# Performance work log

Measured on AMD Instinct MI355X. Metric: run time of the kernel, lower is better.

## Reference

```python
import jax, jax.numpy as jnp
import numpy as np

# PDELayer config (matches torch defaults)
Nx, Ny = 48, 48
Lx, Ly = 1.0, 1.0
T, dt = 0.01, 0.001
dx, dy = Lx / Nx, Ly / Ny
Nt = int(T / dt)  # 10 sequential stencil steps
B = 16384


def setup_inputs() -> dict:
    key = jax.random.key(0)
    u0 = jax.random.normal(key, (B, 1, Nx, Ny), dtype=jnp.float32)
    alpha_w = jnp.array([0.1, 0.1, 0.1], dtype=jnp.float32)  # alpha_w1..3
    beta_w = jnp.array([0.3, 0.2, 0.2], dtype=jnp.float32)   # beta_w1..3
    return {"u0": u0, "alpha_w": alpha_w, "beta_w": beta_w}


def _coeff_grids(alpha_w, beta_w):
    x = jnp.linspace(0.0, Lx, Nx, dtype=jnp.float32)
    y = jnp.linspace(0.0, Ly, Ny, dtype=jnp.float32)
    yy, xx = jnp.meshgrid(y, x, indexing='ij')  # [Ny, Nx]
    two_pi = jnp.float32(2.0 * np.pi)
    alpha_grid = 0.5 * dt * (alpha_w[0]
                             + alpha_w[1] * jnp.sin(two_pi * yy)
                             + alpha_w[2] * jnp.sin(2.0 * two_pi * yy)) / dx ** 2
    beta_grid = dt * (beta_w[0]
                      + beta_w[1] * jnp.cos(two_pi * xx)
                      + beta_w[2] * jnp.cos(2.0 * two_pi * xx)) / dy ** 2
    return alpha_grid[None], beta_grid[None]  # [1, Nx, Ny] (Nx==Ny)


def reference(u0, alpha_w, beta_w):
    alpha_grid, beta_grid = _coeff_grids(alpha_w, beta_w)
    # reflect-pad once; boundary ring stays frozen during time stepping
    u = jnp.pad(u0[:, 0], ((0, 0), (1, 1), (1, 1)), mode='reflect')  # [B, Nx+2, Ny+2]

    def step(u, _):
        ui = u[:, 1:-1, 1:-1]
        u_xx = u[:, 2:, 1:-1] - 2.0 * ui + u[:, :-2, 1:-1]
        u_yy = u[:, 1:-1, 2:] - 2.0 * ui + u[:, 1:-1, :-2]
        u = u.at[:, 1:-1, 1:-1].set(ui + alpha_grid * u_xx + beta_grid * u_yy)
        return u, None

    u, _ = jax.lax.scan(step, u, None, length=Nt)
    return u[:, 1:-1, 1:-1][:, None]  # [B, 1, Nx, Ny]
```

## Files before the change

### kernel.cpp

```cpp
#include <hip/hip_runtime.h>


typedef float v2f __attribute__((ext_vector_type(2)));

constexpr int NXY   = 48;
constexpr int CELLS = NXY * NXY;
constexpr int NT    = 10;
constexpr int TPB   = 64;

__device__ __forceinline__ float dpp_up(float oldv, float src) {
    return __int_as_float(__builtin_amdgcn_update_dpp(
        __float_as_int(oldv), __float_as_int(src), 0x111, 0xF, 0xF, false));
}
__device__ __forceinline__ float dpp_dn(float oldv, float src) {
    return __int_as_float(__builtin_amdgcn_update_dpp(
        __float_as_int(oldv), __float_as_int(src), 0x101, 0xF, 0xF, false));
}

__global__ __launch_bounds__(TPB)
__attribute__((amdgpu_waves_per_eu(2, 4)))
void pde_heat_kernel(
    const float* __restrict__ u0,
    const float* __restrict__ aw,
    const float* __restrict__ bw,
    float* __restrict__ out)
{
    const int lane = threadIdx.x;
    const int img  = blockIdx.x;
    const int r = lane & 15;
    const int c = lane >> 4;
    const float4* __restrict__ u4 = (const float4*)(u0 + (long long)img * CELLS);
    float4*       __restrict__ o4 = (float4*)(out + (long long)img * CELLS);

    const int fb = r * 36 + c * 3;

    v2f v[3][6], w[3][6];
    #pragma unroll
    for (int ii = 0; ii < 3; ++ii)
        #pragma unroll
        for (int k = 0; k < 3; ++k) {
            float4 t = u4[fb + 12 * ii + k];
            v[ii][2*k]   = (v2f){t.x, t.y};
            v[ii][2*k+1] = (v2f){t.z, t.w};
        }

    const float a0 = aw[0], a1 = aw[1], a2 = aw[2];
    const float b0 = bw[0], b1 = bw[1], b2 = bw[2];
    float ca[3];
    #pragma unroll
    for (int ii = 0; ii < 3; ++ii) {
        float y = (float)(3 * r + ii) * (1.0f / 47.0f);
        ca[ii] = 1.152f * (a0 + a1 * __builtin_amdgcn_sinf(y)
                              + a2 * __builtin_amdgcn_sinf(2.0f * y));
    }
    v2f cb2[6];
    #pragma unroll
    for (int k = 0; k < 6; ++k) {
        float x0 = (float)(12 * c + 2 * k)     * (1.0f / 47.0f);
        float x1 = (float)(12 * c + 2 * k + 1) * (1.0f / 47.0f);
        cb2[k].x = 2.304f * (b0 + b1 * __builtin_amdgcn_cosf(x0)
                                + b2 * __builtin_amdgcn_cosf(2.0f * x0));
        cb2[k].y = 2.304f * (b0 + b1 * __builtin_amdgcn_cosf(x1)
                                + b2 * __builtin_amdgcn_cosf(2.0f * x1));
    }
    v2f cc[3][6];
    #pragma unroll
    for (int ii = 0; ii < 3; ++ii) {
        float t = 1.0f - 2.0f * ca[ii];
        #pragma unroll
        for (int k = 0; k < 6; ++k) {
            cc[ii][k].x = t - 2.0f * cb2[k].x;
            cc[ii][k].y = t - 2.0f * cb2[k].y;
        }
    }

    v2f ab[6], hb[6];
    #pragma unroll
    for (int k = 0; k < 6; ++k) { ab[k] = v[1][k]; hb[k] = v[1][k]; }

    float gH[3];
    #pragma unroll
    for (int ii = 0; ii < 3; ++ii) gH[ii] = (c == 0) ? v[ii][0].y : v[ii][5].x;

    const int laneL = lane - 16, laneR = lane + 16;
    const bool cLft = (c == 0), cRgt = (c == 3);

    #pragma unroll
    for (int k = 0; k < 6; ++k) {
        ab[k].x = dpp_up(ab[k].x, v[2][k].x);
        ab[k].y = dpp_up(ab[k].y, v[2][k].y);
        hb[k].x = dpp_dn(hb[k].x, v[0][k].x);
        hb[k].y = dpp_dn(hb[k].y, v[0][k].y);
    }
    float hlp[3], hrp[3];
    #pragma unroll
    for (int ii = 0; ii < 3; ++ii) {
        hlp[ii] = __shfl(v[ii][5].y, laneL);
        hrp[ii] = __shfl(v[ii][0].x, laneR);
    }

    auto cellpair = [&](int ii, int k, const v2f (&rowU)[6], const v2f (&rowM)[6],
                        const v2f (&rowD)[6], float lf, float rt) -> v2f {
        v2f cv = rowM[k];
        v2f s1 = rowU[k] + rowD[k];
        v2f s2;
        s2.x = lf + cv.y;
        s2.y = cv.x + rt;
        return cc[ii][k] * cv + ca[ii] * s1 + cb2[k] * s2;
    };

    auto step = [&](const v2f (&src)[3][6], v2f (&dst)[3][6], bool stage) {
        float hl[3], hr[3];
        #pragma unroll
        for (int ii = 0; ii < 3; ++ii) {
            hl[ii] = cLft ? gH[ii] : hlp[ii];
            hr[ii] = cRgt ? gH[ii] : hrp[ii];
        }
        #pragma unroll
        for (int ii = 0; ii < 3; ++ii) {
            const v2f (&rowU)[6] = (ii == 0) ? ab : src[ii - 1];
            const v2f (&rowD)[6] = (ii == 2) ? hb : src[ii + 1];
            #pragma unroll
            for (int k = 1; k < 5; ++k)
                dst[ii][k] = cellpair(ii, k, rowU, src[ii], rowD,
                                      src[ii][k-1].y, src[ii][k+1].x);
            dst[ii][0] = cellpair(ii, 0, rowU, src[ii], rowD,
                                  hl[ii], src[ii][1].x);
            dst[ii][5] = cellpair(ii, 5, rowU, src[ii], rowD,
                                  src[ii][4].y, hr[ii]);
            if (stage) {
                hlp[ii] = __shfl(dst[ii][5].y, laneL);
                hrp[ii] = __shfl(dst[ii][0].x, laneR);
                if (ii == 2) {
                    #pragma unroll
                    for (int k = 0; k < 6; ++k) {
                        ab[k].x = dpp_up(ab[k].x, dst[2][k].x);
                        ab[k].y = dpp_up(ab[k].y, dst[2][k].y);
                        hb[k].x = dpp_dn(hb[k].x, dst[0][k].x);
                        hb[k].y = dpp_dn(hb[k].y, dst[0][k].y);
                    }
                }
            }
        }
    };

    #pragma unroll
    for (int t = 0; t < NT; ++t) {
        if ((t & 1) == 0) step(v, w, t != NT - 1);
        else              step(w, v, t != NT - 1);
    }

    #pragma unroll
    for (int ii = 0; ii < 3; ++ii)
        #pragma unroll
        for (int k = 0; k < 3; ++k) {
            float4 t;
            t.x = v[ii][2*k].x;   t.y = v[ii][2*k].y;
            t.z = v[ii][2*k+1].x; t.w = v[ii][2*k+1].y;
            o4[fb + 12 * ii + k] = t;
        }
}

extern "C" void kernel_launch(void* const* d_in, const int* in_sizes, int n_in,
                              void* d_out, int out_size, void* d_ws, size_t ws_size,
                              hipStream_t stream) {
    const float* u0 = (const float*)d_in[0];
    const float* aw = (const float*)d_in[1];
    const float* bw = (const float*)d_in[2];
    float* out = (float*)d_out;

    const int B = in_sizes[0] / CELLS;
    pde_heat_kernel<<<B, TPB, 0, stream>>>(u0, aw, bw, out);
}
```

Before: 76.01 us.

## Process two images per block, prefetching the second while computing the first

Each 64-thread block now handles two images. Both are loaded into registers up front so the second image's load overlaps the first image's compute, and the coefficient setup is amortized across both. The time loop is no longer fully unrolled (pairs of steps with unroll 1). The precomputed centre-coefficient array is dropped in favour of computing the Laplacian directly, and the waves-per-EU hint is tightened. This raises register pressure and halves the grid size, which could reduce latency hiding.

```diff
diff --git a/kernel.cpp b/kernel.cpp
--- a/kernel.cpp
+++ b/kernel.cpp
@@ -18,7 +18,7 @@
 }
 
 __global__ __launch_bounds__(TPB)
-__attribute__((amdgpu_waves_per_eu(2, 4)))
+__attribute__((amdgpu_waves_per_eu(2, 3)))
 void pde_heat_kernel(
     const float* __restrict__ u0,
     const float* __restrict__ aw,
@@ -26,22 +26,32 @@
     float* __restrict__ out)
 {
     const int lane = threadIdx.x;
-    const int img  = blockIdx.x;
     const int r = lane & 15;
     const int c = lane >> 4;
-    const float4* __restrict__ u4 = (const float4*)(u0 + (long long)img * CELLS);
-    float4*       __restrict__ o4 = (float4*)(out + (long long)img * CELLS);
+    const long long img0 = (long long)blockIdx.x * 2;
+    const float4* __restrict__ u4a = (const float4*)(u0 + img0 * CELLS);
+    const float4* __restrict__ u4b = u4a + (CELLS / 4);
+    float4*       __restrict__ o4a = (float4*)(out + img0 * CELLS);
+    float4*       __restrict__ o4b = o4a + (CELLS / 4);
 
     const int fb = r * 36 + c * 3;
 
-    v2f v[3][6], w[3][6];
+    v2f A[3][6], B[3][6];
     #pragma unroll
     for (int ii = 0; ii < 3; ++ii)
         #pragma unroll
         for (int k = 0; k < 3; ++k) {
-            float4 t = u4[fb + 12 * ii + k];
-            v[ii][2*k]   = (v2f){t.x, t.y};
-            v[ii][2*k+1] = (v2f){t.z, t.w};
+            float4 t = u4a[fb + 12 * ii + k];
+            A[ii][2*k]   = (v2f){t.x, t.y};
+            A[ii][2*k+1] = (v2f){t.z, t.w};
+        }
+    #pragma unroll
+    for (int ii = 0; ii < 3; ++ii)
+        #pragma unroll
+        for (int k = 0; k < 3; ++k) {
+            float4 t = u4b[fb + 12 * ii + k];
+            B[ii][2*k]   = (v2f){t.x, t.y};
+            B[ii][2*k+1] = (v2f){t.z, t.w};
         }
 
     const float a0 = aw[0], a1 = aw[1], a2 = aw[2];
@@ -63,41 +73,32 @@
         cb2[k].y = 2.304f * (b0 + b1 * __builtin_amdgcn_cosf(x1)
                                 + b2 * __builtin_amdgcn_cosf(2.0f * x1));
     }
-    v2f cc[3][6];
-    #pragma unroll
-    for (int ii = 0; ii < 3; ++ii) {
-        float t = 1.0f - 2.0f * ca[ii];
-        #pragma unroll
-        for (int k = 0; k < 6; ++k) {
-            cc[ii][k].x = t - 2.0f * cb2[k].x;
-            cc[ii][k].y = t - 2.0f * cb2[k].y;
-        }
-    }
 
     v2f ab[6], hb[6];
-    #pragma unroll
-    for (int k = 0; k < 6; ++k) { ab[k] = v[1][k]; hb[k] = v[1][k]; }
-
-    float gH[3];
-    #pragma unroll
-    for (int ii = 0; ii < 3; ++ii) gH[ii] = (c == 0) ? v[ii][0].y : v[ii][5].x;
+    float gH[3], hlp[3], hrp[3];
 
     const int laneL = lane - 16, laneR = lane + 16;
     const bool cLft = (c == 0), cRgt = (c == 3);
 
-    #pragma unroll
-    for (int k = 0; k < 6; ++k) {
-        ab[k].x = dpp_up(ab[k].x, v[2][k].x);
-        ab[k].y = dpp_up(ab[k].y, v[2][k].y);
-        hb[k].x = dpp_dn(hb[k].x, v[0][k].x);
-        hb[k].y = dpp_dn(hb[k].y, v[0][k].y);
-    }
-    float hlp[3], hrp[3];
-    #pragma unroll
-    for (int ii = 0; ii < 3; ++ii) {
-        hlp[ii] = __shfl(v[ii][5].y, laneL);
-        hrp[ii] = __shfl(v[ii][0].x, laneR);
-    }
+    auto prime = [&](const v2f (&u)[3][6]) {
+        #pragma unroll
+        for (int k = 0; k < 6; ++k) { ab[k] = u[1][k]; hb[k] = u[1][k]; }
+        #pragma unroll
+        for (int k = 0; k < 6; ++k) {
+            ab[k].x = dpp_up(ab[k].x, u[2][k].x);
+            ab[k].y = dpp_up(ab[k].y, u[2][k].y);
+            hb[k].x = dpp_dn(hb[k].x, u[0][k].x);
+            hb[k].y = dpp_dn(hb[k].y, u[0][k].y);
+        }
+        #pragma unroll
+        for (int ii = 0; ii < 3; ++ii)
+            gH[ii] = cLft ? u[ii][0].y : u[ii][5].x;
+        #pragma unroll
+        for (int ii = 0; ii < 3; ++ii) {
+            hlp[ii] = __shfl(u[ii][5].y, laneL);
+            hrp[ii] = __shfl(u[ii][0].x, laneR);
+        }
+    };
 
     auto cellpair = [&](int ii, int k, const v2f (&rowU)[6], const v2f (&rowM)[6],
                         const v2f (&rowD)[6], float lf, float rt) -> v2f {
@@ -106,10 +107,12 @@
         v2f s2;
         s2.x = lf + cv.y;
         s2.y = cv.x + rt;
-        return cc[ii][k] * cv + ca[ii] * s1 + cb2[k] * s2;
+        v2f uxx = s1 - 2.0f * cv;
+        v2f uyy = s2 - 2.0f * cv;
+        return cv + ca[ii] * uxx + cb2[k] * uyy;
     };
 
-    auto step = [&](const v2f (&src)[3][6], v2f (&dst)[3][6], bool stage) {
+    auto step = [&](const v2f (&src)[3][6], v2f (&dst)[3][6]) {
         float hl[3], hr[3];
         #pragma unroll
         for (int ii = 0; ii < 3; ++ii) {
@@ -128,37 +131,46 @@
                                   hl[ii], src[ii][1].x);
             dst[ii][5] = cellpair(ii, 5, rowU, src[ii], rowD,
                                   src[ii][4].y, hr[ii]);
-            if (stage) {
-                hlp[ii] = __shfl(dst[ii][5].y, laneL);
-                hrp[ii] = __shfl(dst[ii][0].x, laneR);
-                if (ii == 2) {
-                    #pragma unroll
-                    for (int k = 0; k < 6; ++k) {
-                        ab[k].x = dpp_up(ab[k].x, dst[2][k].x);
-                        ab[k].y = dpp_up(ab[k].y, dst[2][k].y);
-                        hb[k].x = dpp_dn(hb[k].x, dst[0][k].x);
-                        hb[k].y = dpp_dn(hb[k].y, dst[0][k].y);
-                    }
+            hlp[ii] = __shfl(dst[ii][5].y, laneL);
+            hrp[ii] = __shfl(dst[ii][0].x, laneR);
+            if (ii == 2) {
+                #pragma unroll
+                for (int k = 0; k < 6; ++k) {
+                    ab[k].x = dpp_up(ab[k].x, dst[2][k].x);
+                    ab[k].y = dpp_up(ab[k].y, dst[2][k].y);
+                    hb[k].x = dpp_dn(hb[k].x, dst[0][k].x);
+                    hb[k].y = dpp_dn(hb[k].y, dst[0][k].y);
                 }
             }
         }
     };
 
-    #pragma unroll
-    for (int t = 0; t < NT; ++t) {
-        if ((t & 1) == 0) step(v, w, t != NT - 1);
-        else              step(w, v, t != NT - 1);
-    }
+    auto run10 = [&](v2f (&u)[3][6]) {
+        #pragma unroll 1
+        for (int it = 0; it < NT / 2; ++it) {
+            v2f m[3][6];
+            step(u, m);
+            step(m, u);
+        }
+    };
+    auto storeimg = [&](const v2f (&u)[3][6], float4* __restrict__ o4) {
+        #pragma unroll
+        for (int ii = 0; ii < 3; ++ii)
+            #pragma unroll
+            for (int k = 0; k < 3; ++k) {
+                float4 t;
+                t.x = u[ii][2*k].x;   t.y = u[ii][2*k].y;
+                t.z = u[ii][2*k+1].x; t.w = u[ii][2*k+1].y;
+                o4[fb + 12 * ii + k] = t;
+            }
+    };
 
-    #pragma unroll
-    for (int ii = 0; ii < 3; ++ii)
-        #pragma unroll
-        for (int k = 0; k < 3; ++k) {
-            float4 t;
-            t.x = v[ii][2*k].x;   t.y = v[ii][2*k].y;
-            t.z = v[ii][2*k+1].x; t.w = v[ii][2*k+1].y;
-            o4[fb + 12 * ii + k] = t;
-        }
+    prime(A);
+    run10(A);
+    storeimg(A, o4a);
+    prime(B);
+    run10(B);
+    storeimg(B, o4b);
 }
 
 extern "C" void kernel_launch(void* const* d_in, const int* in_sizes, int n_in,
@@ -170,5 +182,5 @@
     float* out = (float*)d_out;
 
     const int B = in_sizes[0] / CELLS;
-    pde_heat_kernel<<<B, TPB, 0, stream>>>(u0, aw, bw, out);
+    pde_heat_kernel<<<B / 2, TPB, 0, stream>>>(u0, aw, bw, out);
 }
```

After: 82.26 us. 1.08x slower.
